# Kernel optimization log

Measured on AMD Instinct MI355X. Metric: run time of the kernel, lower is better.

## Reference

```python
import jax, jax.numpy as jnp
import numpy as np

D = 512
H = 8
W = 128  # window_size
HD = D // H
EPS = 1e-5


def _layernorm(x, g, b):
    mu = jnp.mean(x, axis=-1, keepdims=True)
    var = jnp.mean(jnp.square(x - mu), axis=-1, keepdims=True)
    return (x - mu) * jax.lax.rsqrt(var + EPS) * g + b


def setup_inputs() -> dict:
    key = jax.random.key(0)
    ks = jax.random.split(key, 6)
    B, S = 4, 8192
    src = jax.random.normal(ks[0], (B, S, D), jnp.float32)
    sc = 1.0 / np.sqrt(D)
    in_proj_w = jax.random.normal(ks[1], (3 * D, D), jnp.float32) * sc
    in_proj_b = jnp.zeros((3 * D,), jnp.float32)
    out_w = jax.random.normal(ks[2], (D, D), jnp.float32) * sc
    out_b = jnp.zeros((D,), jnp.float32)
    w1 = jax.random.normal(ks[3], (4 * D, D), jnp.float32) * sc
    b1 = jnp.zeros((4 * D,), jnp.float32)
    w2 = jax.random.normal(ks[4], (D, 4 * D), jnp.float32) * (1.0 / np.sqrt(4 * D))
    b2 = jnp.zeros((D,), jnp.float32)
    return {
        'src': src,
        'in_proj_w': in_proj_w, 'in_proj_b': in_proj_b,
        'out_w': out_w, 'out_b': out_b,
        'ln1_g': jnp.ones((D,), jnp.float32), 'ln1_b': jnp.zeros((D,), jnp.float32),
        'w1': w1, 'b1': b1, 'w2': w2, 'b2': b2,
        'ln2_g': jnp.ones((D,), jnp.float32), 'ln2_b': jnp.zeros((D,), jnp.float32),
    }


def reference(src, in_proj_w, in_proj_b, out_w, out_b, ln1_g, ln1_b,
              w1, b1, w2, b2, ln2_g, ln2_b):
    B, S, _ = src.shape
    nW = S // W
    x = src.reshape(B, nW, W, D)  # block-diagonal windows
    # packed qkv projection (torch MultiheadAttention in_proj)
    qkv = jnp.einsum('bnwd,ed->bnwe', x, in_proj_w) + in_proj_b
    q, k, v = jnp.split(qkv, 3, axis=-1)
    q = q.reshape(B, nW, W, H, HD)
    k = k.reshape(B, nW, W, H, HD)
    v = v.reshape(B, nW, W, H, HD)
    scores = jnp.einsum('bnqhd,bnkhd->bnhqk', q, k) / np.sqrt(HD)
    probs = jax.nn.softmax(scores, axis=-1)
    attn = jnp.einsum('bnhqk,bnkhd->bnqhd', probs, v).reshape(B, nW, W, D)
    attn = jnp.einsum('bnwd,ed->bnwe', attn, out_w) + out_b
    x = _layernorm(x + attn, ln1_g, ln1_b)
    ff = jnp.einsum('bnwf,df->bnwd', jax.nn.relu(jnp.einsum('bnwd,fd->bnwf', x, w1) + b1), w2) + b2
    x = _layernorm(x + ff, ln2_g, ln2_b)
    return x.reshape(B, S, D)
```

## Files before the change

kernel.cpp:

```cpp
#include <hip/hip_runtime.h>
#include <hip/hip_bf16.h>
#include <math.h>

typedef __bf16 bf16;
typedef bf16 bf16x8 __attribute__((ext_vector_type(8)));
typedef bf16 bf16x4 __attribute__((ext_vector_type(4)));
typedef float f32x4 __attribute__((ext_vector_type(4)));

#define MFMA16(a, b, c) __builtin_amdgcn_mfma_f32_16x16x32_bf16(a, b, c, 0, 0, 0)

__device__ __forceinline__ uint32_t swz(uint32_t base, uint32_t row, uint32_t rs, uint32_t cb) {
    return base + row * rs + (((cb >> 4) ^ (row & 7u)) << 4) + (cb & 15u);
}

__device__ __forceinline__ void gload16(const void* g, void* l) {
    __builtin_amdgcn_global_load_lds((const __attribute__((address_space(1))) void*)g,
                                     (__attribute__((address_space(3))) void*)l, 16, 0, 0);
}



__global__ void wcvt_kernel(const float* __restrict__ wqkv, const float* __restrict__ wout,
                            const float* __restrict__ w1f, const float* __restrict__ w2f,
                            bf16* __restrict__ o) {
    int i = blockIdx.x * blockDim.x + threadIdx.x;
    const float* s;
    int soff, doff;
    if (i < 98304) {
        int u = i;
        int tile = u >> 11, c = (u >> 9) & 3, nn = u & 511;
        int n = (tile >> 4) * 512 + nn;
        int k = (tile & 15) * 32 + c * 8;
        s = wqkv; soff = n * 512 + k; doff = u * 8;
    } else if (i < 131072) {
        int u = i - 98304;
        int tile = u >> 11, c = (u >> 9) & 3, nn = u & 511;
        int k = tile * 32 + c * 8;
        s = wout; soff = nn * 512 + k; doff = 786432 + u * 8;
    } else if (i < 262144) {
        int u = i - 131072;
        int tile = u >> 11, c = (u >> 9) & 3, nn = u & 511;
        int n = (tile >> 4) * 512 + nn;
        int k = (tile & 15) * 32 + c * 8;
        s = w1f; soff = n * 512 + k; doff = 1048576 + u * 8;
    } else {
        int u = i - 262144;
        int t = u >> 11, c = (u >> 9) & 3, nn = u & 511;
        int k = t * 32 + c * 8;
        s = w2f; soff = nn * 2048 + k; doff = 2097152 + u * 8;
    }
    float4 v0 = *(const float4*)(s + soff);
    float4 v1 = *(const float4*)(s + soff + 4);
    bf16x8 h = { (bf16)v0.x, (bf16)v0.y, (bf16)v0.z, (bf16)v0.w,
                 (bf16)v1.x, (bf16)v1.y, (bf16)v1.z, (bf16)v1.w };
    *(bf16x8*)(o + doff) = h;
}

__global__ void xcvt_kernel(float* __restrict__ src) {
    int row = blockIdx.x * 4 + (threadIdx.x >> 6);
    int l = threadIdx.x & 63;
    float* rp = src + (size_t)row * 512 + l * 8;
    float4 v0 = *(const float4*)rp;
    float4 v1 = *(const float4*)(rp + 4);
    asm volatile("s_waitcnt vmcnt(0)" ::: "memory");
    bf16x8 h = { (bf16)v0.x, (bf16)v0.y, (bf16)v0.z, (bf16)v0.w,
                 (bf16)v1.x, (bf16)v1.y, (bf16)v1.z, (bf16)v1.w };
    *(bf16x8*)((bf16*)(src + (size_t)row * 512) + l * 8) = h;
}

#define PHASED_LOOP(NT)                                                                \
    int ib = 0;                                                                        \
    _Pragma("unroll 1")                                                                \
    for (int t = 0; t < (NT); ++t) {                                                   \
        int in2 = ib + 2; if (in2 >= 3) in2 -= 3;                                      \
        const uint32_t A0 = (uint32_t)ib * 8192u;                                      \
        const uint32_t B0 = 24576u + (uint32_t)ib * 32768u;                            \
        bf16x8 a[4], b[8];                                                             \
                                                                \
        _Pragma("unroll")                                                              \
        for (int i = 0; i < 4; ++i)                                                    \
            a[i] = *(const bf16x8*)(smem + A0 + quad * 2048 + (wm * 64 + i * 16 + l16) * 16); \
        _Pragma("unroll")                                                              \
        for (int nt = 0; nt < 4; ++nt)                                                 \
            b[nt] = *(const bf16x8*)(smem + B0 + quad * 8192 + (wn * 128 + nt * 16 + l16) * 16); \
        if (t + 2 < (NT)) { STAGE_A(in2, t + 2); STAGE_B(in2, t + 2, 0); }             \
        __builtin_amdgcn_s_barrier();                                                  \
        asm volatile("s_waitcnt lgkmcnt(0)" ::: "memory");                             \
        __builtin_amdgcn_sched_barrier(0);                                             \
        __builtin_amdgcn_s_setprio(1);                                                 \
        _Pragma("unroll")                                                              \
        for (int nt = 0; nt < 4; ++nt)                                                 \
            _Pragma("unroll")                                                          \
            for (int i = 0; i < 4; ++i) acc[i][nt] = MFMA16(a[i], b[nt], acc[i][nt]);  \
        __builtin_amdgcn_s_setprio(0);                                                 \
        __builtin_amdgcn_s_barrier();                                                  \
                                                                \
        _Pragma("unroll")                                                              \
        for (int nt = 4; nt < 8; ++nt)                                                 \
            b[nt] = *(const bf16x8*)(smem + B0 + quad * 8192 + (wn * 128 + nt * 16 + l16) * 16); \
        if (t + 2 < (NT)) { STAGE_B(in2, t + 2, 1); STAGE_B(in2, t + 2, 2); STAGE_B(in2, t + 2, 3); } \
        __builtin_amdgcn_s_barrier();                                                  \
        asm volatile("s_waitcnt lgkmcnt(0)" ::: "memory");                             \
        __builtin_amdgcn_sched_barrier(0);                                             \
        __builtin_amdgcn_s_setprio(1);                                                 \
        _Pragma("unroll")                                                              \
        for (int nt = 4; nt < 8; ++nt)                                                 \
            _Pragma("unroll")                                                          \
            for (int i = 0; i < 4; ++i) acc[i][nt] = MFMA16(a[i], b[nt], acc[i][nt]);  \
        __builtin_amdgcn_s_setprio(0);                                                 \
        if (t + 2 < (NT)) asm volatile("s_waitcnt vmcnt(5)" ::: "memory");             \
        else              asm volatile("s_waitcnt vmcnt(0)" ::: "memory");             \
        __builtin_amdgcn_s_barrier();                                                  \
        ib = (ib == 2) ? 0 : ib + 1;                                                   \
    }

extern "C" __global__ __launch_bounds__(512, 2)
void qkv_kernel(const char* __restrict__ xb, const char* __restrict__ Wqkvp,
                const float* __restrict__ bqkv, char* __restrict__ qOb,
                char* __restrict__ kvb) {
    extern __shared__ char smem[];
    const int tid = threadIdx.x;
    const int w = tid >> 6, lane = tid & 63, l16 = lane & 15, quad = lane >> 4;
    const int wm = w >> 2, wn = w & 3;
    const int mb = blockIdx.x, cb = blockIdx.y;

    f32x4 acc[4][8];
#pragma unroll
    for (int i = 0; i < 4; ++i)
#pragma unroll
        for (int nt = 0; nt < 8; ++nt) acc[i][nt] = (f32x4){0.f, 0.f, 0.f, 0.f};

#define STAGE_A(ib_, t_)                                                               \
    {                                                                                  \
        int ca = w >> 1, rg = w & 1;                                                   \
        gload16(xb + (size_t)(mb * 128 + rg * 64 + lane) * 2048 + (t_) * 64 + ca * 16, \
                smem + (uint32_t)(ib_) * 8192u + ca * 2048 + rg * 1024);               \
    }
#define STAGE_B(ib_, t_, j_)                                                           \
    {                                                                                  \
        int idx = w * 4 + (j_), c = idx >> 3, ng = idx & 7;                            \
        gload16(Wqkvp + (size_t)(cb * 16 + (t_)) * 32768 + c * 8192 + ng * 1024 + lane * 16, \
                smem + 24576u + (uint32_t)(ib_) * 32768u + (uint32_t)c * 8192 + (uint32_t)ng * 1024); \
    }

    STAGE_A(0, 0); STAGE_B(0, 0, 0); STAGE_B(0, 0, 1); STAGE_B(0, 0, 2); STAGE_B(0, 0, 3);
    STAGE_A(1, 1); STAGE_B(1, 1, 0); STAGE_B(1, 1, 1); STAGE_B(1, 1, 2); STAGE_B(1, 1, 3);
    asm volatile("s_waitcnt vmcnt(5)" ::: "memory");
    __builtin_amdgcn_s_barrier();

    PHASED_LOOP(16)
#undef STAGE_A
#undef STAGE_B

    const uint32_t sb = 24576u + (uint32_t)w * 4096u;
#pragma unroll
    for (int i = 0; i < 4; ++i) {
#pragma unroll
        for (int nt = 0; nt < 8; ++nt) {
            float bb = bqkv[cb * 512 + wn * 128 + nt * 16 + l16];
#pragma unroll
            for (int r = 0; r < 4; ++r)
                *(bf16*)(smem + swz(sb, quad * 4 + r, 256, (nt * 16 + l16) * 2)) =
                    (bf16)(acc[i][nt][r] + bb);
        }
        asm volatile("s_waitcnt lgkmcnt(0)" ::: "memory");
#pragma unroll
        for (int j = 0; j < 4; ++j) {
            int uu = j * 64 + lane;
            int row = uu >> 4, ch = uu & 15;
            bf16x8 v = *(bf16x8*)(smem + swz(sb, row, 256, ch * 16));
            size_t row_g = (size_t)(mb * 128 + wm * 64 + i * 16 + row);
            int nb2 = wn * 256 + ch * 16;
            if (cb == 0)      *(bf16x8*)(qOb + row_g * 1024 + nb2) = v;
            else if (cb == 1) *(bf16x8*)(kvb + row_g * 2048 + nb2) = v;
            else              *(bf16x8*)(kvb + row_g * 2048 + 1024 + nb2) = v;
        }
        asm volatile("s_waitcnt lgkmcnt(0)" ::: "memory");
    }
}

#define AVT 0u
#define ASCR 16384u
extern "C" __global__ __launch_bounds__(512, 4)
void attn_kernel(char* __restrict__ qOb, const char* __restrict__ kvb) {
    extern __shared__ char smem[];
    const int tid = threadIdx.x;
    const int wid = tid >> 6, lane = tid & 63, l16 = lane & 15, quad = lane >> 4;
    const int win = blockIdx.x >> 3, head = blockIdx.x & 7;
    const size_t wrow0 = (size_t)win * 128;
    f32x4 zero4 = { 0.f, 0.f, 0.f, 0.f };

    {
        int key = tid >> 2, d0 = (tid & 3) * 16;
        const char* vs = kvb + (wrow0 + key) * 2048 + 1024 + head * 128 + d0 * 2;
#pragma unroll
        for (int j = 0; j < 2; ++j) {
            bf16x8 v = *(const bf16x8*)(vs + j * 16);
#pragma unroll
            for (int e = 0; e < 8; ++e)
                *(bf16*)(smem + swz(AVT, d0 + j * 8 + e, 256, key * 2)) = v[e];
        }
    }
    __syncthreads();

    bf16x8 qf[2];
#pragma unroll
    for (int ks = 0; ks < 2; ++ks)
        qf[ks] = *(const bf16x8*)(qOb + (wrow0 + wid * 16 + l16) * 1024 + head * 128 + ks * 64 + quad * 16);

    f32x4 sa[8];
#pragma unroll
    for (int nt = 0; nt < 8; ++nt) sa[nt] = zero4;
#pragma unroll
    for (int nt = 0; nt < 8; ++nt)
#pragma unroll
        for (int ks = 0; ks < 2; ++ks) {
            bf16x8 kb = *(const bf16x8*)(kvb + (wrow0 + nt * 16 + l16) * 2048 + head * 128 + ks * 64 + quad * 16);
            sa[nt] = MFMA16(qf[ks], kb, sa[nt]);
        }
#pragma unroll
    for (int nt = 0; nt < 8; ++nt) sa[nt] *= 0.125f;
#pragma unroll
    for (int r = 0; r < 4; ++r) {
        float m = sa[0][r];
#pragma unroll
        for (int nt = 1; nt < 8; ++nt) m = fmaxf(m, sa[nt][r]);
#pragma unroll
        for (int sft = 1; sft < 16; sft <<= 1) m = fmaxf(m, __shfl_xor(m, sft, 64));
        float s = 0.f;
#pragma unroll
        for (int nt = 0; nt < 8; ++nt) {
            float e = __expf(sa[nt][r] - m);
            sa[nt][r] = e;
            s += e;
        }
#pragma unroll
        for (int sft = 1; sft < 16; sft <<= 1) s += __shfl_xor(s, sft, 64);
        float inv = 1.0f / s;
#pragma unroll
        for (int nt = 0; nt < 8; ++nt) sa[nt][r] *= inv;
    }

    const uint32_t sb = ASCR + (uint32_t)wid * 2048;
    bf16x8 pf[4];
#pragma unroll
    for (int hf = 0; hf < 2; ++hf) {
#pragma unroll
        for (int nt = 0; nt < 4; ++nt)
#pragma unroll
            for (int r = 0; r < 4; ++r)
                *(bf16*)(smem + swz(sb, quad * 4 + r, 128, (nt * 16 + l16) * 2)) = (bf16)sa[hf * 4 + nt][r];
        asm volatile("s_waitcnt lgkmcnt(0)" ::: "memory");
#pragma unroll
        for (int ks = 0; ks < 2; ++ks)
            pf[hf * 2 + ks] = *(bf16x8*)(smem + swz(sb, l16, 128, ks * 64 + quad * 16));
        asm volatile("s_waitcnt lgkmcnt(0)" ::: "memory");
    }

    f32x4 ov[4];
#pragma unroll
    for (int nt = 0; nt < 4; ++nt) {
        ov[nt] = zero4;
#pragma unroll
        for (int ks = 0; ks < 4; ++ks) {
            bf16x8 vb = *(bf16x8*)(smem + swz(AVT, nt * 16 + l16, 256, ks * 64 + quad * 16));
            ov[nt] = MFMA16(pf[ks], vb, ov[nt]);
        }
    }
#pragma unroll
    for (int hf = 0; hf < 2; ++hf) {
#pragma unroll
        for (int nt = 0; nt < 2; ++nt)
#pragma unroll
            for (int r = 0; r < 4; ++r)
                *(bf16*)(smem + swz(sb, quad * 4 + r, 128, (nt * 16 + l16) * 2)) = (bf16)ov[hf * 2 + nt][r];
        asm volatile("s_waitcnt lgkmcnt(0)" ::: "memory");
        {
            int row = lane >> 2, ch = lane & 3;
            bf16x8 v = *(bf16x8*)(smem + swz(sb, row, 128, ch * 16));
            *(bf16x8*)(qOb + (wrow0 + wid * 16 + row) * 1024 + head * 128 + hf * 64 + ch * 16) = v;
        }
        asm volatile("s_waitcnt lgkmcnt(0)" ::: "memory");
    }
}

extern "C" __global__ __launch_bounds__(512, 2)
void outproj_kernel(char* __restrict__ srcb, const char* __restrict__ qOb,
                    const char* __restrict__ Woutp, const float* __restrict__ bout,
                    const float* __restrict__ g1, const float* __restrict__ be1) {
    extern __shared__ char smem[];
    const int tid = threadIdx.x;
    const int w = tid >> 6, lane = tid & 63, l16 = lane & 15, quad = lane >> 4;
    const int wm = w >> 2, wn = w & 3;
    const int mb = blockIdx.x;

    f32x4 acc[4][8];
#pragma unroll
    for (int i = 0; i < 4; ++i)
#pragma unroll
        for (int nt = 0; nt < 8; ++nt) acc[i][nt] = (f32x4){0.f, 0.f, 0.f, 0.f};

#define STAGE_A(ib_, t_)                                                               \
    {                                                                                  \
        int ca = w >> 1, rg = w & 1;                                                   \
        gload16(qOb + (size_t)(mb * 128 + rg * 64 + lane) * 1024 + (t_) * 64 + ca * 16, \
                smem + (uint32_t)(ib_) * 8192u + ca * 2048 + rg * 1024);               \
    }
#define STAGE_B(ib_, t_, j_)                                                           \
    {                                                                                  \
        int idx = w * 4 + (j_), c = idx >> 3, ng = idx & 7;                            \
        gload16(Woutp + (size_t)(t_) * 32768 + c * 8192 + ng * 1024 + lane * 16,       \
                smem + 24576u + (uint32_t)(ib_) * 32768u + (uint32_t)c * 8192 + (uint32_t)ng * 1024); \
    }

    STAGE_A(0, 0); STAGE_B(0, 0, 0); STAGE_B(0, 0, 1); STAGE_B(0, 0, 2); STAGE_B(0, 0, 3);
    STAGE_A(1, 1); STAGE_B(1, 1, 0); STAGE_B(1, 1, 1); STAGE_B(1, 1, 2); STAGE_B(1, 1, 3);
    asm volatile("s_waitcnt vmcnt(5)" ::: "memory");
    __builtin_amdgcn_s_barrier();

    PHASED_LOOP(16)
#undef STAGE_A
#undef STAGE_B

#pragma unroll
    for (int nt = 0; nt < 8; ++nt) {
        int col = wn * 128 + nt * 16 + l16;
        float bb = bout[col];
#pragma unroll
        for (int i = 0; i < 4; ++i)
#pragma unroll
            for (int r = 0; r < 4; ++r) {
                int row = mb * 128 + wm * 64 + i * 16 + quad * 4 + r;
                float xv = (float)*(const bf16*)(srcb + (size_t)row * 2048 + col * 2);
                acc[i][nt][r] += bb + xv;
            }
    }
    float ps[4][4], ps2[4][4];
#pragma unroll
    for (int i = 0; i < 4; ++i)
#pragma unroll
        for (int r = 0; r < 4; ++r) {
            float s = 0.f, s2 = 0.f;
#pragma unroll
            for (int nt = 0; nt < 8; ++nt) {
                float v = acc[i][nt][r];
                s += v;
                s2 += v * v;
            }
#pragma unroll
            for (int sft = 1; sft < 16; sft <<= 1) {
                s += __shfl_xor(s, sft, 64);
                s2 += __shfl_xor(s2, sft, 64);
            }
            ps[i][r] = s;
            ps2[i][r] = s2;
        }
    if (l16 == 0) {
#pragma unroll
        for (int i = 0; i < 4; ++i)
#pragma unroll
            for (int r = 0; r < 4; ++r) {
                int row_l = wm * 64 + i * 16 + quad * 4 + r;
                *(float*)(smem + row_l * 32 + wn * 8) = ps[i][r];
                *(float*)(smem + row_l * 32 + wn * 8 + 4) = ps2[i][r];
            }
    }
    __syncthreads();
    const uint32_t sb = 24576u + (uint32_t)w * 4096u;
#pragma unroll
    for (int i = 0; i < 4; ++i) {
#pragma unroll
        for (int r = 0; r < 4; ++r) {
            int row_l = wm * 64 + i * 16 + quad * 4 + r;
            float S = 0.f, S2 = 0.f;
#pragma unroll
            for (int w4 = 0; w4 < 4; ++w4) {
                S += *(const float*)(smem + row_l * 32 + w4 * 8);
                S2 += *(const float*)(smem + row_l * 32 + w4 * 8 + 4);
            }
            float mu = S * (1.0f / 512.0f);
            float var = S2 * (1.0f / 512.0f) - mu * mu;
            float rstd = rsqrtf(var + 1e-5f);
#pragma unroll
            for (int nt = 0; nt < 8; ++nt) {
                int col = wn * 128 + nt * 16 + l16;
                float v = (acc[i][nt][r] - mu) * rstd * g1[col] + be1[col];
                *(bf16*)(smem + swz(sb, quad * 4 + r, 256, (nt * 16 + l16) * 2)) = (bf16)v;
            }
        }
        asm volatile("s_waitcnt lgkmcnt(0)" ::: "memory");
#pragma unroll
        for (int j = 0; j < 4; ++j) {
            int uu = j * 64 + lane;
            int row = uu >> 4, ch = uu & 15;
            bf16x8 v = *(bf16x8*)(smem + swz(sb, row, 256, ch * 16));
            *(bf16x8*)(srcb + (size_t)(mb * 128 + wm * 64 + i * 16 + row) * 2048 + 1024 +
                       wn * 256 + ch * 16) = v;
        }
        asm volatile("s_waitcnt lgkmcnt(0)" ::: "memory");
    }
}

extern "C" __global__ __launch_bounds__(512, 2)
void ff1_kernel(char* __restrict__ srcb, const char* __restrict__ W1p,
                const float* __restrict__ b1, char* __restrict__ doutb,
                char* __restrict__ wsOb) {
    extern __shared__ char smem[];
    const int tid = threadIdx.x;
    const int w = tid >> 6, lane = tid & 63, l16 = lane & 15, quad = lane >> 4;
    const int wm = w >> 2, wn = w & 3;
    const int mb = blockIdx.x, cb = blockIdx.y;

    f32x4 acc[4][8];
#pragma unroll
    for (int i = 0; i < 4; ++i)
#pragma unroll
        for (int nt = 0; nt < 8; ++nt) acc[i][nt] = (f32x4){0.f, 0.f, 0.f, 0.f};

#define STAGE_A(ib_, t_)                                                               \
    {                                                                                  \
        int ca = w >> 1, rg = w & 1;                                                   \
        gload16(srcb + (size_t)(mb * 128 + rg * 64 + lane) * 2048 + 1024 + (t_) * 64 + ca * 16, \
                smem + (uint32_t)(ib_) * 8192u + ca * 2048 + rg * 1024);               \
    }
#define STAGE_B(ib_, t_, j_)                                                           \
    {                                                                                  \
        int idx = w * 4 + (j_), c = idx >> 3, ng = idx & 7;                            \
        gload16(W1p + (size_t)(cb * 16 + (t_)) * 32768 + c * 8192 + ng * 1024 + lane * 16, \
                smem + 24576u + (uint32_t)(ib_) * 32768u + (uint32_t)c * 8192 + (uint32_t)ng * 1024); \
    }

    STAGE_A(0, 0); STAGE_B(0, 0, 0); STAGE_B(0, 0, 1); STAGE_B(0, 0, 2); STAGE_B(0, 0, 3);
    STAGE_A(1, 1); STAGE_B(1, 1, 0); STAGE_B(1, 1, 1); STAGE_B(1, 1, 2); STAGE_B(1, 1, 3);
    asm volatile("s_waitcnt vmcnt(5)" ::: "memory");
    __builtin_amdgcn_s_barrier();

    PHASED_LOOP(16)
#undef STAGE_A
#undef STAGE_B

    const uint32_t sb = 24576u + (uint32_t)w * 4096u;
#pragma unroll
    for (int i = 0; i < 4; ++i) {
#pragma unroll
        for (int nt = 0; nt < 8; ++nt) {
            float bb = b1[cb * 512 + wn * 128 + nt * 16 + l16];
#pragma unroll
            for (int r = 0; r < 4; ++r)
                *(bf16*)(smem + swz(sb, quad * 4 + r, 256, (nt * 16 + l16) * 2)) =
                    (bf16)fmaxf(acc[i][nt][r] + bb, 0.0f);
        }
        asm volatile("s_waitcnt lgkmcnt(0)" ::: "memory");
#pragma unroll
        for (int j = 0; j < 4; ++j) {
            int uu = j * 64 + lane;
            int row = uu >> 4, ch = uu & 15;
            bf16x8 v = *(bf16x8*)(smem + swz(sb, row, 256, ch * 16));
            size_t row_g = (size_t)(mb * 128 + wm * 64 + i * 16 + row);
            int nb2 = wn * 256 + ch * 16;
            if (cb < 2)       *(bf16x8*)(doutb + row_g * 2048 + cb * 1024 + nb2) = v;
            else if (cb == 2) *(bf16x8*)(srcb + row_g * 2048 + nb2) = v;
            else              *(bf16x8*)(wsOb + row_g * 1024 + nb2) = v;
        }
        asm volatile("s_waitcnt lgkmcnt(0)" ::: "memory");
    }
}

extern "C" __global__ __launch_bounds__(512, 2)
void ff2_kernel(char* __restrict__ doutb, const char* __restrict__ srcb,
                const char* __restrict__ wsOb, const char* __restrict__ W2p,
                const float* __restrict__ b2, const float* __restrict__ g2,
                const float* __restrict__ be2) {
    extern __shared__ char smem[];
    const int tid = threadIdx.x;
    const int w = tid >> 6, lane = tid & 63, l16 = lane & 15, quad = lane >> 4;
    const int wm = w >> 2, wn = w & 3;
    const int mb = blockIdx.x;

    f32x4 acc[4][8];
#pragma unroll
    for (int i = 0; i < 4; ++i)
#pragma unroll
        for (int nt = 0; nt < 8; ++nt) acc[i][nt] = (f32x4){0.f, 0.f, 0.f, 0.f};

#define STAGE_A(ib_, t_)                                                               \
    {                                                                                  \
        const char* hb; int rstride, koffb;                                            \
        if ((t_) < 32)      { hb = doutb; rstride = 2048; koffb = (t_) * 64; }         \
        else if ((t_) < 48) { hb = srcb;  rstride = 2048; koffb = ((t_) - 32) * 64; }  \
        else                { hb = wsOb;  rstride = 1024; koffb = ((t_) - 48) * 64; }  \
        int ca = w >> 1, rg = w & 1;                                                   \
        gload16(hb + (size_t)(mb * 128 + rg * 64 + lane) * rstride + koffb + ca * 16,  \
                smem + (uint32_t)(ib_) * 8192u + ca * 2048 + rg * 1024);               \
    }
#define STAGE_B(ib_, t_, j_)                                                           \
    {                                                                                  \
        int idx = w * 4 + (j_), c = idx >> 3, ng = idx & 7;                            \
        gload16(W2p + (size_t)(t_) * 32768 + c * 8192 + ng * 1024 + lane * 16,         \
                smem + 24576u + (uint32_t)(ib_) * 32768u + (uint32_t)c * 8192 + (uint32_t)ng * 1024); \
    }

    STAGE_A(0, 0); STAGE_B(0, 0, 0); STAGE_B(0, 0, 1); STAGE_B(0, 0, 2); STAGE_B(0, 0, 3);
    STAGE_A(1, 1); STAGE_B(1, 1, 0); STAGE_B(1, 1, 1); STAGE_B(1, 1, 2); STAGE_B(1, 1, 3);
    asm volatile("s_waitcnt vmcnt(5)" ::: "memory");
    __builtin_amdgcn_s_barrier();

    PHASED_LOOP(64)
#undef STAGE_A
#undef STAGE_B

#pragma unroll
    for (int nt = 0; nt < 8; ++nt) {
        int col = wn * 128 + nt * 16 + l16;
        float bb = b2[col];
#pragma unroll
        for (int i = 0; i < 4; ++i)
#pragma unroll
            for (int r = 0; r < 4; ++r) {
                int row = mb * 128 + wm * 64 + i * 16 + quad * 4 + r;
                float x1v = (float)*(const bf16*)(srcb + (size_t)row * 2048 + 1024 + col * 2);
                acc[i][nt][r] += bb + x1v;
            }
    }
    float ps[4][4], ps2[4][4];
#pragma unroll
    for (int i = 0; i < 4; ++i)
#pragma unroll
        for (int r = 0; r < 4; ++r) {
            float s = 0.f, s2 = 0.f;
#pragma unroll
            for (int nt = 0; nt < 8; ++nt) {
                float v = acc[i][nt][r];
                s += v;
                s2 += v * v;
            }
#pragma unroll
            for (int sft = 1; sft < 16; sft <<= 1) {
                s += __shfl_xor(s, sft, 64);
                s2 += __shfl_xor(s2, sft, 64);
            }
            ps[i][r] = s;
            ps2[i][r] = s2;
        }
    if (l16 == 0) {
#pragma unroll
        for (int i = 0; i < 4; ++i)
#pragma unroll
            for (int r = 0; r < 4; ++r) {
                int row_l = wm * 64 + i * 16 + quad * 4 + r;
                *(float*)(smem + row_l * 32 + wn * 8) = ps[i][r];
                *(float*)(smem + row_l * 32 + wn * 8 + 4) = ps2[i][r];
            }
    }
    __syncthreads();
#pragma unroll
    for (int i = 0; i < 4; ++i)
#pragma unroll
        for (int r = 0; r < 4; ++r) {
            int row_l = wm * 64 + i * 16 + quad * 4 + r;
            float S = 0.f, S2 = 0.f;
#pragma unroll
            for (int w4 = 0; w4 < 4; ++w4) {
                S += *(const float*)(smem + row_l * 32 + w4 * 8);
                S2 += *(const float*)(smem + row_l * 32 + w4 * 8 + 4);
            }
            float mu = S * (1.0f / 512.0f);
            float var = S2 * (1.0f / 512.0f) - mu * mu;
            float rstd = rsqrtf(var + 1e-5f);
            size_t row = (size_t)(mb * 128 + row_l);
#pragma unroll
            for (int nt = 0; nt < 8; ++nt) {
                int col = wn * 128 + nt * 16 + l16;
                *(float*)(doutb + row * 2048 + col * 4) =
                    (acc[i][nt][r] - mu) * rstd * g2[col] + be2[col];
            }
        }
}

extern "C" void kernel_launch(void* const* d_in, const int* in_sizes, int n_in,
                              void* d_out, int out_size, void* d_ws, size_t ws_size,
                              hipStream_t stream) {
    (void)in_sizes; (void)n_in; (void)out_size; (void)ws_size;
    float* src = (float*)d_in[0];
    const float* ipw = (const float*)d_in[1];
    const float* ipb = (const float*)d_in[2];
    const float* ow  = (const float*)d_in[3];
    const float* ob  = (const float*)d_in[4];
    const float* g1  = (const float*)d_in[5];
    const float* be1 = (const float*)d_in[6];
    const float* w1  = (const float*)d_in[7];
    const float* b1  = (const float*)d_in[8];
    const float* w2  = (const float*)d_in[9];
    const float* b2  = (const float*)d_in[10];
    const float* g2  = (const float*)d_in[11];
    const float* be2 = (const float*)d_in[12];
    bf16* ws = (bf16*)d_ws;
    char* srcb = (char*)src;
    char* doutb = (char*)d_out;
    char* qOb = (char*)d_ws + 6291456;

    wcvt_kernel<<<1536, 256, 0, stream>>>(ipw, ow, w1, w2, ws);
    xcvt_kernel<<<8192, 256, 0, stream>>>(src);

    hipFuncSetAttribute((const void*)qkv_kernel, hipFuncAttributeMaxDynamicSharedMemorySize, 122880);
    hipFuncSetAttribute((const void*)attn_kernel, hipFuncAttributeMaxDynamicSharedMemorySize, 32768);
    hipFuncSetAttribute((const void*)outproj_kernel, hipFuncAttributeMaxDynamicSharedMemorySize, 122880);
    hipFuncSetAttribute((const void*)ff1_kernel, hipFuncAttributeMaxDynamicSharedMemorySize, 122880);
    hipFuncSetAttribute((const void*)ff2_kernel, hipFuncAttributeMaxDynamicSharedMemorySize, 122880);

    qkv_kernel<<<dim3(256, 3), 512, 122880, stream>>>(srcb, (const char*)ws, ipb, qOb, doutb);
    attn_kernel<<<2048, 512, 32768, stream>>>(qOb, doutb);
    outproj_kernel<<<256, 512, 122880, stream>>>(srcb, qOb, (const char*)(ws + 786432), ob, g1, be1);
    ff1_kernel<<<dim3(256, 4), 512, 122880, stream>>>(srcb, (const char*)(ws + 1048576), b1, doutb, qOb);
    ff2_kernel<<<256, 512, 122880, stream>>>(doutb, srcb, qOb, (const char*)(ws + 2097152), b2, g2, be2);
}
```

Before: 505.5 us.

## Halve N-tile width of QKV and FF1 GEMMs to raise occupancy

Shrinks the output column tile of the QKV and FF1 GEMMs from 512 to 256. The weight repacking, the LDS staging, the accumulator count and the epilogue stores all change to match the narrower tile, and the grid gets twice as many column blocks. LDS drops to 72KB and launch bounds now request 4 blocks per CU, aiming for more waves in flight and better latency hiding. In exchange each A tile is loaded twice as often, arithmetic intensity per block falls, and the simpler single-phase loop drops the phased interleaving of MFMA with staging.

```diff
diff --git a/kernel.cpp b/kernel.cpp
--- a/kernel.cpp
+++ b/kernel.cpp
@@ -28,8 +28,8 @@
     int soff, doff;
     if (i < 98304) {
         int u = i;
-        int tile = u >> 11, c = (u >> 9) & 3, nn = u & 511;
-        int n = (tile >> 4) * 512 + nn;
+        int tile = u >> 10, c = (u >> 8) & 3, nn = u & 255;
+        int n = (tile >> 4) * 256 + nn;
         int k = (tile & 15) * 32 + c * 8;
         s = wqkv; soff = n * 512 + k; doff = u * 8;
     } else if (i < 131072) {
@@ -39,8 +39,8 @@
         s = wout; soff = nn * 512 + k; doff = 786432 + u * 8;
     } else if (i < 262144) {
         int u = i - 131072;
-        int tile = u >> 11, c = (u >> 9) & 3, nn = u & 511;
-        int n = (tile >> 4) * 512 + nn;
+        int tile = u >> 10, c = (u >> 8) & 3, nn = u & 255;
+        int n = (tile >> 4) * 256 + nn;
         int k = (tile & 15) * 32 + c * 8;
         s = w1f; soff = n * 512 + k; doff = 1048576 + u * 8;
     } else {
@@ -68,6 +68,31 @@
     *(bf16x8*)((bf16*)(src + (size_t)row * 512) + l * 8) = h;
 }
 
+#define N256_LOOP(NT)                                                                  \
+    int ib = 0;                                                                        \
+    _Pragma("unroll 1")                                                                \
+    for (int t = 0; t < (NT); ++t) {                                                   \
+        int in2 = ib + 2; if (in2 >= 3) in2 -= 3;                                      \
+        const uint32_t A0 = (uint32_t)ib * 8192u;                                      \
+        const uint32_t B0 = 24576u + (uint32_t)ib * 16384u;                            \
+        bf16x8 a[4], b[4];                                                             \
+        _Pragma("unroll")                                                              \
+        for (int i = 0; i < 4; ++i)                                                    \
+            a[i] = *(const bf16x8*)(smem + A0 + quad * 2048 + (wm * 64 + i * 16 + l16) * 16); \
+        _Pragma("unroll")                                                              \
+        for (int nt = 0; nt < 4; ++nt)                                                 \
+            b[nt] = *(const bf16x8*)(smem + B0 + quad * 4096 + (wn * 64 + nt * 16 + l16) * 16); \
+        if (t + 2 < (NT)) { STAGE_A(in2, t + 2); STAGE_B2(in2, t + 2, 0); STAGE_B2(in2, t + 2, 1); } \
+        _Pragma("unroll")                                                              \
+        for (int nt = 0; nt < 4; ++nt)                                                 \
+            _Pragma("unroll")                                                          \
+            for (int i = 0; i < 4; ++i) acc[i][nt] = MFMA16(a[i], b[nt], acc[i][nt]);  \
+        if (t + 2 < (NT)) asm volatile("s_waitcnt vmcnt(3)" ::: "memory");             \
+        else              asm volatile("s_waitcnt vmcnt(0)" ::: "memory");             \
+        __builtin_amdgcn_s_barrier();                                                  \
+        ib = (ib == 2) ? 0 : ib + 1;                                                   \
+    }
+
 #define PHASED_LOOP(NT)                                                                \
     int ib = 0;                                                                        \
     _Pragma("unroll 1")                                                                \
@@ -114,7 +139,7 @@
         ib = (ib == 2) ? 0 : ib + 1;                                                   \
     }
 
-extern "C" __global__ __launch_bounds__(512, 2)
+extern "C" __global__ __launch_bounds__(512, 4)
 void qkv_kernel(const char* __restrict__ xb, const char* __restrict__ Wqkvp,
                 const float* __restrict__ bqkv, char* __restrict__ qOb,
                 char* __restrict__ kvb) {
@@ -124,11 +149,11 @@
     const int wm = w >> 2, wn = w & 3;
     const int mb = blockIdx.x, cb = blockIdx.y;
 
-    f32x4 acc[4][8];
+    f32x4 acc[4][4];
 #pragma unroll
     for (int i = 0; i < 4; ++i)
 #pragma unroll
-        for (int nt = 0; nt < 8; ++nt) acc[i][nt] = (f32x4){0.f, 0.f, 0.f, 0.f};
+        for (int nt = 0; nt < 4; ++nt) acc[i][nt] = (f32x4){0.f, 0.f, 0.f, 0.f};
 
 #define STAGE_A(ib_, t_)                                                               \
     {                                                                                  \
@@ -136,44 +161,43 @@
         gload16(xb + (size_t)(mb * 128 + rg * 64 + lane) * 2048 + (t_) * 64 + ca * 16, \
                 smem + (uint32_t)(ib_) * 8192u + ca * 2048 + rg * 1024);               \
     }
-#define STAGE_B(ib_, t_, j_)                                                           \
-    {                                                                                  \
-        int idx = w * 4 + (j_), c = idx >> 3, ng = idx & 7;                            \
-        gload16(Wqkvp + (size_t)(cb * 16 + (t_)) * 32768 + c * 8192 + ng * 1024 + lane * 16, \
-                smem + 24576u + (uint32_t)(ib_) * 32768u + (uint32_t)c * 8192 + (uint32_t)ng * 1024); \
-    }
-
-    STAGE_A(0, 0); STAGE_B(0, 0, 0); STAGE_B(0, 0, 1); STAGE_B(0, 0, 2); STAGE_B(0, 0, 3);
-    STAGE_A(1, 1); STAGE_B(1, 1, 0); STAGE_B(1, 1, 1); STAGE_B(1, 1, 2); STAGE_B(1, 1, 3);
-    asm volatile("s_waitcnt vmcnt(5)" ::: "memory");
+#define STAGE_B2(ib_, t_, j_)                                                          \
+    {                                                                                  \
+        int idx = w * 2 + (j_), c = idx >> 2, ng = idx & 3;                            \
+        gload16(Wqkvp + (size_t)(cb * 16 + (t_)) * 16384 + c * 4096 + ng * 1024 + lane * 16, \
+                smem + 24576u + (uint32_t)(ib_) * 16384u + (uint32_t)c * 4096 + (uint32_t)ng * 1024); \
+    }
+
+    STAGE_A(0, 0); STAGE_B2(0, 0, 0); STAGE_B2(0, 0, 1);
+    STAGE_A(1, 1); STAGE_B2(1, 1, 0); STAGE_B2(1, 1, 1);
+    asm volatile("s_waitcnt vmcnt(3)" ::: "memory");
     __builtin_amdgcn_s_barrier();
 
-    PHASED_LOOP(16)
+    N256_LOOP(16)
 #undef STAGE_A
-#undef STAGE_B
-
-    const uint32_t sb = 24576u + (uint32_t)w * 4096u;
+#undef STAGE_B2
+
+    const uint32_t sb = 24576u + (uint32_t)w * 2048u;
 #pragma unroll
     for (int i = 0; i < 4; ++i) {
 #pragma unroll
-        for (int nt = 0; nt < 8; ++nt) {
-            float bb = bqkv[cb * 512 + wn * 128 + nt * 16 + l16];
+        for (int nt = 0; nt < 4; ++nt) {
+            float bb = bqkv[cb * 256 + wn * 64 + nt * 16 + l16];
 #pragma unroll
             for (int r = 0; r < 4; ++r)
-                *(bf16*)(smem + swz(sb, quad * 4 + r, 256, (nt * 16 + l16) * 2)) =
+                *(bf16*)(smem + swz(sb, quad * 4 + r, 128, (nt * 16 + l16) * 2)) =
                     (bf16)(acc[i][nt][r] + bb);
         }
         asm volatile("s_waitcnt lgkmcnt(0)" ::: "memory");
 #pragma unroll
-        for (int j = 0; j < 4; ++j) {
-            int uu = j * 64 + lane;
-            int row = uu >> 4, ch = uu & 15;
-            bf16x8 v = *(bf16x8*)(smem + swz(sb, row, 256, ch * 16));
+        for (int t2 = 0; t2 < 2; ++t2) {
+            int row = t2 * 8 + (lane >> 3), ch = lane & 7;
+            bf16x8 v = *(bf16x8*)(smem + swz(sb, row, 128, ch * 16));
             size_t row_g = (size_t)(mb * 128 + wm * 64 + i * 16 + row);
-            int nb2 = wn * 256 + ch * 16;
-            if (cb == 0)      *(bf16x8*)(qOb + row_g * 1024 + nb2) = v;
-            else if (cb == 1) *(bf16x8*)(kvb + row_g * 2048 + nb2) = v;
-            else              *(bf16x8*)(kvb + row_g * 2048 + 1024 + nb2) = v;
+            int cbyte = wn * 128 + ch * 16;
+            if (cb < 2)      *(bf16x8*)(qOb + row_g * 1024 + cb * 512 + cbyte) = v;
+            else if (cb < 4) *(bf16x8*)(kvb + row_g * 2048 + (cb - 2) * 512 + cbyte) = v;
+            else             *(bf16x8*)(kvb + row_g * 2048 + 1024 + (cb - 4) * 512 + cbyte) = v;
         }
         asm volatile("s_waitcnt lgkmcnt(0)" ::: "memory");
     }
@@ -401,7 +425,7 @@
     }
 }
 
-extern "C" __global__ __launch_bounds__(512, 2)
+extern "C" __global__ __launch_bounds__(512, 4)
 void ff1_kernel(char* __restrict__ srcb, const char* __restrict__ W1p,
                 const float* __restrict__ b1, char* __restrict__ doutb,
                 char* __restrict__ wsOb) {
@@ -411,11 +435,11 @@
     const int wm = w >> 2, wn = w & 3;
     const int mb = blockIdx.x, cb = blockIdx.y;
 
-    f32x4 acc[4][8];
+    f32x4 acc[4][4];
 #pragma unroll
     for (int i = 0; i < 4; ++i)
 #pragma unroll
-        for (int nt = 0; nt < 8; ++nt) acc[i][nt] = (f32x4){0.f, 0.f, 0.f, 0.f};
+        for (int nt = 0; nt < 4; ++nt) acc[i][nt] = (f32x4){0.f, 0.f, 0.f, 0.f};
 
 #define STAGE_A(ib_, t_)                                                               \
     {                                                                                  \
@@ -423,44 +447,43 @@
         gload16(srcb + (size_t)(mb * 128 + rg * 64 + lane) * 2048 + 1024 + (t_) * 64 + ca * 16, \
                 smem + (uint32_t)(ib_) * 8192u + ca * 2048 + rg * 1024);               \
     }
-#define STAGE_B(ib_, t_, j_)                                                           \
-    {                                                                                  \
-        int idx = w * 4 + (j_), c = idx >> 3, ng = idx & 7;                            \
-        gload16(W1p + (size_t)(cb * 16 + (t_)) * 32768 + c * 8192 + ng * 1024 + lane * 16, \
-                smem + 24576u + (uint32_t)(ib_) * 32768u + (uint32_t)c * 8192 + (uint32_t)ng * 1024); \
-    }
-
-    STAGE_A(0, 0); STAGE_B(0, 0, 0); STAGE_B(0, 0, 1); STAGE_B(0, 0, 2); STAGE_B(0, 0, 3);
-    STAGE_A(1, 1); STAGE_B(1, 1, 0); STAGE_B(1, 1, 1); STAGE_B(1, 1, 2); STAGE_B(1, 1, 3);
-    asm volatile("s_waitcnt vmcnt(5)" ::: "memory");
+#define STAGE_B2(ib_, t_, j_)                                                          \
+    {                                                                                  \
+        int idx = w * 2 + (j_), c = idx >> 2, ng = idx & 3;                            \
+        gload16(W1p + (size_t)(cb * 16 + (t_)) * 16384 + c * 4096 + ng * 1024 + lane * 16, \
+                smem + 24576u + (uint32_t)(ib_) * 16384u + (uint32_t)c * 4096 + (uint32_t)ng * 1024); \
+    }
+
+    STAGE_A(0, 0); STAGE_B2(0, 0, 0); STAGE_B2(0, 0, 1);
+    STAGE_A(1, 1); STAGE_B2(1, 1, 0); STAGE_B2(1, 1, 1);
+    asm volatile("s_waitcnt vmcnt(3)" ::: "memory");
     __builtin_amdgcn_s_barrier();
 
-    PHASED_LOOP(16)
+    N256_LOOP(16)
 #undef STAGE_A
-#undef STAGE_B
-
-    const uint32_t sb = 24576u + (uint32_t)w * 4096u;
+#undef STAGE_B2
+
+    const uint32_t sb = 24576u + (uint32_t)w * 2048u;
 #pragma unroll
     for (int i = 0; i < 4; ++i) {
 #pragma unroll
-        for (int nt = 0; nt < 8; ++nt) {
-            float bb = b1[cb * 512 + wn * 128 + nt * 16 + l16];
+        for (int nt = 0; nt < 4; ++nt) {
+            float bb = b1[cb * 256 + wn * 64 + nt * 16 + l16];
 #pragma unroll
             for (int r = 0; r < 4; ++r)
-                *(bf16*)(smem + swz(sb, quad * 4 + r, 256, (nt * 16 + l16) * 2)) =
+                *(bf16*)(smem + swz(sb, quad * 4 + r, 128, (nt * 16 + l16) * 2)) =
                     (bf16)fmaxf(acc[i][nt][r] + bb, 0.0f);
         }
         asm volatile("s_waitcnt lgkmcnt(0)" ::: "memory");
 #pragma unroll
-        for (int j = 0; j < 4; ++j) {
-            int uu = j * 64 + lane;
-            int row = uu >> 4, ch = uu & 15;
-            bf16x8 v = *(bf16x8*)(smem + swz(sb, row, 256, ch * 16));
+        for (int t2 = 0; t2 < 2; ++t2) {
+            int row = t2 * 8 + (lane >> 3), ch = lane & 7;
+            bf16x8 v = *(bf16x8*)(smem + swz(sb, row, 128, ch * 16));
             size_t row_g = (size_t)(mb * 128 + wm * 64 + i * 16 + row);
-            int nb2 = wn * 256 + ch * 16;
-            if (cb < 2)       *(bf16x8*)(doutb + row_g * 2048 + cb * 1024 + nb2) = v;
-            else if (cb == 2) *(bf16x8*)(srcb + row_g * 2048 + nb2) = v;
-            else              *(bf16x8*)(wsOb + row_g * 1024 + nb2) = v;
+            int cbyte = wn * 128 + ch * 16;
+            if (cb < 4)      *(bf16x8*)(doutb + row_g * 2048 + cb * 512 + cbyte) = v;
+            else if (cb < 6) *(bf16x8*)(srcb + row_g * 2048 + (cb - 4) * 512 + cbyte) = v;
+            else             *(bf16x8*)(wsOb + row_g * 1024 + (cb - 6) * 512 + cbyte) = v;
         }
         asm volatile("s_waitcnt lgkmcnt(0)" ::: "memory");
     }
@@ -602,15 +625,15 @@
     wcvt_kernel<<<1536, 256, 0, stream>>>(ipw, ow, w1, w2, ws);
     xcvt_kernel<<<8192, 256, 0, stream>>>(src);
 
-    hipFuncSetAttribute((const void*)qkv_kernel, hipFuncAttributeMaxDynamicSharedMemorySize, 122880);
+    hipFuncSetAttribute((const void*)qkv_kernel, hipFuncAttributeMaxDynamicSharedMemorySize, 73728);
     hipFuncSetAttribute((const void*)attn_kernel, hipFuncAttributeMaxDynamicSharedMemorySize, 32768);
     hipFuncSetAttribute((const void*)outproj_kernel, hipFuncAttributeMaxDynamicSharedMemorySize, 122880);
-    hipFuncSetAttribute((const void*)ff1_kernel, hipFuncAttributeMaxDynamicSharedMemorySize, 122880);
+    hipFuncSetAttribute((const void*)ff1_kernel, hipFuncAttributeMaxDynamicSharedMemorySize, 73728);
     hipFuncSetAttribute((const void*)ff2_kernel, hipFuncAttributeMaxDynamicSharedMemorySize, 122880);
 
-    qkv_kernel<<<dim3(256, 3), 512, 122880, stream>>>(srcb, (const char*)ws, ipb, qOb, doutb);
+    qkv_kernel<<<dim3(256, 6), 512, 73728, stream>>>(srcb, (const char*)ws, ipb, qOb, doutb);
     attn_kernel<<<2048, 512, 32768, stream>>>(qOb, doutb);
     outproj_kernel<<<256, 512, 122880, stream>>>(srcb, qOb, (const char*)(ws + 786432), ob, g1, be1);
-    ff1_kernel<<<dim3(256, 4), 512, 122880, stream>>>(srcb, (const char*)(ws + 1048576), b1, doutb, qOb);
+    ff1_kernel<<<dim3(256, 8), 512, 73728, stream>>>(srcb, (const char*)(ws + 1048576), b1, doutb, qOb);
     ff2_kernel<<<256, 512, 122880, stream>>>(doutb, srcb, qOb, (const char*)(ws + 2097152), b2, g2, be2);
 }
```

New measurement: 490.1 us. 1.03x faster.
